# Optimization experiments

Measured on AMD Instinct MI355X. Metric: run time of the kernel, lower is better.

Reference implementation:

```python
import jax, jax.numpy as jnp
import numpy as np

V, E, SH, H = 30000, 1024, 2048, 1024   # vocab, emb_size, ses_hid_size, hid_size
B, T = 64, 50
PAD = 10003
H2 = 2 * H  # GRU hidden size


def setup_inputs() -> dict:
    key = jax.random.key(0)
    ks = jax.random.split(key, 12)
    s = 0.02
    emb_W = jax.random.normal(ks[2], (V, E), jnp.float32) * s
    emb_W = emb_W.at[PAD].set(0.0)  # padding_idx row is zero
    return {
        "ses_encoding": jax.random.normal(ks[0], (B, 1, SH), jnp.float32),
        "x": jax.random.randint(ks[1], (B, T), 0, V),
        "emb_W": emb_W,
        "gru_Wih": jax.random.normal(ks[3], (3 * H2, E), jnp.float32) * s,
        "gru_Whh": jax.random.normal(ks[4], (3 * H2, H2), jnp.float32) * s,
        "gru_bih": jax.random.normal(ks[5], (3 * H2,), jnp.float32) * s,
        "gru_bhh": jax.random.normal(ks[6], (3 * H2,), jnp.float32) * s,
        "lin1_W": jax.random.normal(ks[7], (H, SH), jnp.float32) * s,
        "lin1_b": jax.random.normal(ks[8], (H,), jnp.float32) * s,
        "lin2_W": jax.random.normal(ks[9], (E, H2), jnp.float32) * s,
        "lin2_b": jax.random.normal(ks[10], (E,), jnp.float32) * s,
        "out_W": jax.random.normal(ks[11], (V, E), jnp.float32) * s,
    }


def reference(ses_encoding, x, emb_W, gru_Wih, gru_Whh, gru_bih, gru_bhh,
              lin1_W, lin1_b, lin2_W, lin2_b, out_W):
    # ses_encoding: [B,1,SH] -> tanh(lin1) -> [B,1,H] -> view [1,B,H] -> [B,H]
    ses = jnp.tanh(jnp.einsum('bos,hs->boh', ses_encoding, lin1_W) + lin1_b)
    ses_enc = ses.reshape(B, H)  # [B, H]

    toks = x.T  # [T, B], teacher-forced inputs
    tok_next = jnp.concatenate([x[:, 1:], jnp.zeros((B, 1), x.dtype)], axis=1).T  # [T, B]
    has_next = jnp.arange(T) < (T - 1)  # [T]

    def step(h, xs):
        tok, nxt, hn = xs  # tok: [B]
        emb = jnp.where((tok == PAD)[:, None], 0.0, emb_W[tok])  # [B, E] (dropout=eval identity)
        hcat = jnp.concatenate([h, ses_enc], axis=-1)  # [B, 2H]
        gi = emb @ gru_Wih.T + gru_bih    # [B, 6H]
        gh = hcat @ gru_Whh.T + gru_bhh   # [B, 6H]
        i_r, i_z, i_n = jnp.split(gi, 3, axis=-1)
        h_r, h_z, h_n = jnp.split(gh, 3, axis=-1)
        r = jax.nn.sigmoid(i_r + h_r)
        z = jax.nn.sigmoid(i_z + h_z)
        n = jnp.tanh(i_n + r * h_n)
        h_full = (1.0 - z) * n + z * hcat     # [B, 2H]
        h_next = h_full[:, :H]                # keep first hid_size half
        hid_o = h_full @ lin2_W.T + lin2_b + emb  # [B, E]
        logits = hid_o @ out_W.T              # [B, V]
        logp = jax.nn.log_softmax(logits, axis=-1)
        ll = jnp.where(hn, logp[jnp.arange(B), nxt], 0.0)  # [B]
        return h_next, (logits, ll)

    _, (all_logits, all_ll) = jax.lax.scan(step, ses_enc, (toks, tok_next, has_next))
    dec_o = jnp.transpose(all_logits, (1, 0, 2))  # [B, T, V]
    log_l = jnp.sum(all_ll, axis=0)               # [B]
    return dec_o, log_l
```

## Files before the change

### kernel.cpp

```cpp
#include <hip/hip_runtime.h>
#include <hip/hip_bf16.h>
#include <stdint.h>

#define VV   30000
#define EE   1024
#define SHH  2048
#define HH   1024
#define H2   2048
#define G3   6144
#define BB   64
#define TT   50
#define PADT 10003
#define MM   3200
#define NPAD 30080
#define RBLK 64
#define PNB  (NPAD / 64)

typedef __bf16 bf16;
typedef bf16  bf16x8 __attribute__((ext_vector_type(8)));
typedef bf16  bf16x4v __attribute__((ext_vector_type(4)));
typedef float f32x4 __attribute__((ext_vector_type(4)));

__device__ __forceinline__ void async16(void* lds_base, const void* gsrc) {
    __builtin_amdgcn_global_load_lds(
        (const __attribute__((address_space(1))) void*)gsrc,
        (__attribute__((address_space(3))) void*)lds_base, 16, 0, 0);
}

__device__ __forceinline__ int xcd_swizzle(int lin, int nwg) {
    int q = nwg >> 3, r = nwg & 7;
    int x = lin & 7, o = lin >> 3;
    return (x < r ? x * (q + 1) : r * (q + 1) + (x - r) * q) + o;
}

__device__ __forceinline__ float sigmoidf_(float x) {
    return 1.f / (1.f + __expf(-x));
}

__global__ __launch_bounds__(256) void k_conv(bf16* dst, const float* src, int n) {
    int i = (blockIdx.x * 256 + threadIdx.x) * 4;
    if (i + 3 >= n) return;
    float4 v = *(const float4*)&src[i];
    bf16x4v o; o[0] = (bf16)v.x; o[1] = (bf16)v.y; o[2] = (bf16)v.z; o[3] = (bf16)v.w;
    *(bf16x4v*)&dst[i] = o;
}

__global__ __launch_bounds__(256) void k_conv_outw(bf16* dst, const float* src) {
    int row = blockIdx.x;
    int c = threadIdx.x * 4;
    bf16x4v o;
    if (row < VV) {
        float4 v = *(const float4*)&src[(size_t)row * EE + c];
        o[0] = (bf16)v.x; o[1] = (bf16)v.y; o[2] = (bf16)v.z; o[3] = (bf16)v.w;
    } else {
        o[0] = (bf16)0.f; o[1] = (bf16)0.f; o[2] = (bf16)0.f; o[3] = (bf16)0.f;
    }
    *(bf16x4v*)&dst[(size_t)row * EE + c] = o;
}

__global__ __launch_bounds__(256) void k_conv_whhhi(bf16* dst, const float* whh) {
    int d = blockIdx.x;
    int cblk = d / 192, rem = d % 192, g = rem / 64, s = rem % 64;
    const float* srow = whh + (size_t)(g * H2 + 1024 + cblk * 64 + s) * H2;
    int c = threadIdx.x * 4;
    float4 v = *(const float4*)&srow[c];
    bf16x4v o; o[0] = (bf16)v.x; o[1] = (bf16)v.y; o[2] = (bf16)v.z; o[3] = (bf16)v.w;
    *(bf16x4v*)&dst[(size_t)d * HH + c] = o;
}

__global__ __launch_bounds__(256) void k_embed(const int* x, const float* embW, bf16* out) {
    int i = blockIdx.x;
    int t = i >> 6, b = i & 63;
    int tok = x[b * TT + t];
    int e = threadIdx.x * 4;
    bf16x4v o;
    if (tok == PADT) {
        o[0] = (bf16)0.f; o[1] = (bf16)0.f; o[2] = (bf16)0.f; o[3] = (bf16)0.f;
    } else {
        float4 v = *(const float4*)&embW[(size_t)tok * EE + e];
        o[0] = (bf16)v.x; o[1] = (bf16)v.y; o[2] = (bf16)v.z; o[3] = (bf16)v.w;
    }
    *(bf16x4v*)&out[(size_t)i * EE + e] = o;
}

template<int KIND>
__global__ __launch_bounds__(256)
void sgemm64(const float* __restrict__ A, const float* __restrict__ Bm,
             const float* __restrict__ bias, float* __restrict__ Of, bf16* __restrict__ Ob,
             int N, int K, int lda, int ldb, int koff, int ldo) {
    int n0 = blockIdx.x * 64;
    int tid = threadIdx.x;
    int tr = tid >> 4, tc = tid & 15;
    __shared__ float As[64][33];
    __shared__ float Bs[64][33];
    float acc[4][4] = {};
    for (int k0 = 0; k0 < K; k0 += 32) {
        #pragma unroll
        for (int q = 0; q < 8; ++q) {
            int p = q * 256 + tid; int r = p >> 5, kk = p & 31;
            As[r][kk] = A[(size_t)r * lda + k0 + kk];
            Bs[r][kk] = Bm[(size_t)(n0 + r) * ldb + koff + k0 + kk];
        }
        __syncthreads();
        #pragma unroll
        for (int kk = 0; kk < 32; ++kk) {
            float a4[4], b4[4];
            #pragma unroll
            for (int i = 0; i < 4; i++) a4[i] = As[tr * 4 + i][kk];
            #pragma unroll
            for (int j = 0; j < 4; j++) b4[j] = Bs[tc * 4 + j][kk];
            #pragma unroll
            for (int i = 0; i < 4; i++)
                #pragma unroll
                for (int j = 0; j < 4; j++) acc[i][j] += a4[i] * b4[j];
        }
        __syncthreads();
    }
    #pragma unroll
    for (int i = 0; i < 4; i++)
        #pragma unroll
        for (int j = 0; j < 4; j++) {
            int row = tr * 4 + i, col = n0 + tc * 4 + j;
            float v = acc[i][j] + bias[col];
            if (KIND == 0) {
                v = tanhf(v);
                Of[(size_t)row * N + col] = v;
                Ob[(size_t)row * ldo + col] = (bf16)v;
            } else {
                Of[(size_t)row * N + col] = v;
            }
        }
}

template<int KIND>
__global__ __launch_bounds__(256)
void gemm128(const bf16* __restrict__ A, const bf16* __restrict__ Bm,
             void* __restrict__ Cout, const float* __restrict__ bias,
             const bf16* __restrict__ addend, float* __restrict__ pm,
             float* __restrict__ ps, int N, int K, int lda, int ldb, int Nreal) {
    int nwg = gridDim.x * gridDim.y;
    int lin = blockIdx.y * gridDim.x + blockIdx.x;
    int wg = xcd_swizzle(lin, nwg);
    int bx = wg % gridDim.x, by = wg / gridDim.x;
    const int n0 = bx * 128;
    const int m0 = by * 128;
    const int tid = threadIdx.x;
    const int w = tid >> 6, l = tid & 63;
    const int wr = w >> 1, wc = w & 1;
    __shared__ bf16 As[128 * 32];
    __shared__ bf16 Bs[128 * 32];
    f32x4 acc[4][4] = {};
    const int lrow = l >> 2;
    const int lk = (l & 3) * 8;
    for (int kt = 0; kt < K; kt += 32) {
        #pragma unroll
        for (int q = 0; q < 2; ++q) {
            int ch = w * 2 + q;
            async16(&As[ch * 512], A + (size_t)(m0 + ch * 16 + lrow) * lda + kt + lk);
            async16(&Bs[ch * 512], Bm + (size_t)(n0 + ch * 16 + lrow) * ldb + kt + lk);
        }
        __syncthreads();
        bf16x8 af[4], bfr[4];
        #pragma unroll
        for (int mi = 0; mi < 4; mi++)
            af[mi] = *(const bf16x8*)&As[(wr * 64 + mi * 16 + (l & 15)) * 32 + (l >> 4) * 8];
        #pragma unroll
        for (int ni = 0; ni < 4; ni++)
            bfr[ni] = *(const bf16x8*)&Bs[(wc * 64 + ni * 16 + (l & 15)) * 32 + (l >> 4) * 8];
        #pragma unroll
        for (int mi = 0; mi < 4; mi++)
            #pragma unroll
            for (int ni = 0; ni < 4; ni++)
                acc[mi][ni] = __builtin_amdgcn_mfma_f32_16x16x32_bf16(af[mi], bfr[ni], acc[mi][ni], 0, 0, 0);
        __syncthreads();
    }
    #pragma unroll
    for (int mi = 0; mi < 4; mi++)
        #pragma unroll
        for (int ni = 0; ni < 4; ni++) {
            int row0 = m0 + wr * 64 + mi * 16 + (l >> 4) * 4;
            int col = n0 + wc * 64 + ni * 16 + (l & 15);
            f32x4 v = acc[mi][ni];
            #pragma unroll
            for (int r = 0; r < 4; r++) {
                int rr = row0 + r;
                float xv = v[r];
                if constexpr (KIND == 0 || KIND == 1) xv += bias[col];
                if constexpr (KIND == 1) xv += (float)addend[(size_t)rr * N + col];
                if constexpr (KIND == 2) {
                    if (col < Nreal) {
                        int t = rr >> 6, b = rr & 63;
                        ((float*)Cout)[((size_t)(b * TT + t)) * VV + col] = xv;
                    }
                } else {
                    ((bf16*)Cout)[(size_t)rr * N + col] = (bf16)xv;
                }
            }
        }
    if constexpr (KIND == 2) {
        #pragma unroll
        for (int mi = 0; mi < 4; mi++) {
            #pragma unroll
            for (int r = 0; r < 4; r++) {
                float m = -1e30f, s = 0.f;
                #pragma unroll
                for (int ni = 0; ni < 4; ni++) {
                    int col = n0 + wc * 64 + ni * 16 + (l & 15);
                    if (col < Nreal) {
                        float v = acc[mi][ni][r];
                        float M = fmaxf(m, v);
                        s = s * __expf(m - M) + __expf(v - M);
                        m = M;
                    }
                }
                #pragma unroll
                for (int off = 1; off < 16; off <<= 1) {
                    float m2 = __shfl_xor(m, off);
                    float s2 = __shfl_xor(s, off);
                    float M = fmaxf(m, m2);
                    s = s * __expf(m - M) + s2 * __expf(m2 - M);
                    m = M;
                }
                if ((l & 15) == 0) {
                    int row = m0 + wr * 64 + mi * 16 + (l >> 4) * 4 + r;
                    size_t pidx = (size_t)row * PNB + (n0 >> 6) + wc;
                    pm[pidx] = m; ps[pidx] = s;
                }
            }
        }
    }
}

__global__ __launch_bounds__(384, 1)
void k_rnn(const float* __restrict__ Whh,
           const bf16* __restrict__ gi_b,
           const float* __restrict__ ghs,
           bf16* __restrict__ hfx,
           uint32_t* __restrict__ ctr) {
    const int blk = blockIdx.x;
    const int c0 = blk * 16;
    const int tid = threadIdx.x;
    const int wv = tid >> 6;
    const int l  = tid & 63;
    const int g  = wv >> 1;
    const int mh = wv & 1;
    const int lc = l & 15, lk = l >> 4;
    __shared__ float ghl[3][64][17];

    bf16x8 breg[32];
    {
        const float* wrow = Whh + ((size_t)(g * H2 + c0 + lc)) * H2;
        #pragma unroll
        for (int kt = 0; kt < 32; ++kt) {
            const float* p = wrow + kt * 32 + lk * 8;
            float4 v0 = *(const float4*)p;
            float4 v1 = *(const float4*)(p + 4);
            bf16x8 o;
            o[0] = (bf16)v0.x; o[1] = (bf16)v0.y; o[2] = (bf16)v0.z; o[3] = (bf16)v0.w;
            o[4] = (bf16)v1.x; o[5] = (bf16)v1.y; o[6] = (bf16)v1.z; o[7] = (bf16)v1.w;
            breg[kt] = o;
        }
    }
    float pr[8], pz[8], pn[8];
    if (g == 0) {
        #pragma unroll
        for (int j = 0; j < 8; ++j) {
            int b = mh * 32 + lk * 8 + j;
            size_t base = (size_t)b * G3 + c0 + lc;
            pr[j] = ghs[base];
            pz[j] = ghs[base + H2];
            pn[j] = ghs[base + 2 * H2];
        }
    }

    for (int t = 0; t < TT; ++t) {
        const bf16* arow = hfx + ((size_t)t * BB) * H2;
        bf16 qr[8], qz[8], qn[8];
        if (g == 0) {
            const bf16* gp = gi_b + ((size_t)t * BB) * G3;
            #pragma unroll
            for (int j = 0; j < 8; ++j) {
                int b = mh * 32 + lk * 8 + j;
                size_t base = (size_t)b * G3 + c0 + lc;
                qr[j] = gp[base];
                qz[j] = gp[base + H2];
                qn[j] = gp[base + 2 * H2];
            }
        }
        f32x4 acc0 = {}, acc1 = {};
        #pragma unroll
        for (int kt = 0; kt < 32; ++kt) {
            bf16x8 a0 = *(const bf16x8*)(arow + (size_t)(mh * 32 + lc) * H2 + kt * 32 + lk * 8);
            bf16x8 a1 = *(const bf16x8*)(arow + (size_t)(mh * 32 + 16 + lc) * H2 + kt * 32 + lk * 8);
            acc0 = __builtin_amdgcn_mfma_f32_16x16x32_bf16(a0, breg[kt], acc0, 0, 0, 0);
            acc1 = __builtin_amdgcn_mfma_f32_16x16x32_bf16(a1, breg[kt], acc1, 0, 0, 0);
        }
        #pragma unroll
        for (int r = 0; r < 4; ++r) {
            ghl[g][mh * 32 + lk * 4 + r][lc]      = acc0[r];
            ghl[g][mh * 32 + 16 + lk * 4 + r][lc] = acc1[r];
        }
        __syncthreads();
        if (g == 0) {
            #pragma unroll
            for (int j = 0; j < 8; ++j) {
                int b = mh * 32 + lk * 8 + j;
                float hr = ghl[0][b][lc] + pr[j];
                float hz = ghl[1][b][lc] + pz[j];
                float hn = ghl[2][b][lc] + pn[j];
                float rg = sigmoidf_((float)qr[j] + hr);
                float zg = sigmoidf_((float)qz[j] + hz);
                float ng = tanhf((float)qn[j] + rg * hn);
                float hv = (float)arow[(size_t)b * H2 + c0 + lc];
                float hf = (1.f - zg) * ng + zg * hv;
                hfx[((size_t)(t + 1) * BB + b) * H2 + c0 + lc] = (bf16)hf;
            }
        }
        if (t != TT - 1) {
            __syncthreads();
            if (tid == 0) {
                __hip_atomic_fetch_add(&ctr[t], 1u, __ATOMIC_RELEASE, __HIP_MEMORY_SCOPE_AGENT);
                while (__hip_atomic_load(&ctr[t], __ATOMIC_ACQUIRE, __HIP_MEMORY_SCOPE_AGENT) < RBLK)
                    __builtin_amdgcn_s_sleep(1);
            }
            __syncthreads();
        }
    }
}

__global__ __launch_bounds__(256)
void k_hi(const bf16* __restrict__ hfx_,
          const float* __restrict__ ses_f,
          const bf16* __restrict__ Wrh,
          const bf16* __restrict__ gi_b,
          const float* __restrict__ ghs,
          bf16* __restrict__ hfx_out) {
    const int cblk = blockIdx.x;
    const int t    = blockIdx.y;
    const int tid = threadIdx.x;
    const int w = tid >> 6, l = tid & 63;
    __shared__ bf16 As[64 * 32];
    __shared__ bf16 Bs[192 * 32];
    f32x4 acc[12] = {};
    const int lrow = l >> 2;
    const int lk = (l & 3) * 8;
    const bf16* Abase = hfx_ + ((size_t)t * BB) * H2;
    for (int kt = 0; kt < HH; kt += 32) {
        async16(&As[w * 512], Abase + (size_t)(w * 16 + lrow) * H2 + kt + lk);
        #pragma unroll
        for (int q = 0; q < 3; ++q) {
            int cb = w * 3 + q;
            async16(&Bs[cb * 512], Wrh + (size_t)(cblk * 192 + cb * 16 + lrow) * HH + kt + lk);
        }
        __syncthreads();
        bf16x8 af = *(const bf16x8*)&As[(w * 16 + (l & 15)) * 32 + (l >> 4) * 8];
        #pragma unroll
        for (int j = 0; j < 12; j++) {
            bf16x8 bfj = *(const bf16x8*)&Bs[(j * 16 + (l & 15)) * 32 + (l >> 4) * 8];
            acc[j] = __builtin_amdgcn_mfma_f32_16x16x32_bf16(af, bfj, acc[j], 0, 0, 0);
        }
        __syncthreads();
    }
    #pragma unroll
    for (int jc = 0; jc < 4; jc++) {
        int ch = cblk * 64 + jc * 16 + (l & 15);
        #pragma unroll
        for (int r = 0; r < 4; r++) {
            int b = w * 16 + (l >> 4) * 4 + r;
            size_t gb = (size_t)(t * BB + b) * G3 + 1024 + ch;
            size_t sb = (size_t)b * G3 + 1024 + ch;
            float gr = (float)gi_b[gb];
            float gz = (float)gi_b[gb + H2];
            float gn = (float)gi_b[gb + 2 * H2];
            float hr = acc[jc][r]     + ghs[sb];
            float hz = acc[4 + jc][r] + ghs[sb + H2];
            float hn = acc[8 + jc][r] + ghs[sb + 2 * H2];
            float rg = sigmoidf_(gr + hr);
            float zg = sigmoidf_(gz + hz);
            float ng = tanhf(gn + rg * hn);
            float hv = ses_f[b * HH + ch];
            float hf = (1.f - zg) * ng + zg * hv;
            hfx_out[((size_t)(t + 1) * BB + b) * H2 + HH + ch] = (bf16)hf;
        }
    }
}

__global__ void k_lse(const float* __restrict__ pm, const float* __restrict__ ps,
                      const float* __restrict__ logits, const int* __restrict__ x,
                      float* __restrict__ ll) {
    int row = blockIdx.x;
    int t = row >> 6, b = row & 63;
    int l = threadIdx.x;
    float m = -1e30f, s = 0.f;
    for (int i = l; i < PNB; i += 64) {
        float mi = pm[(size_t)row * PNB + i];
        float si = ps[(size_t)row * PNB + i];
        float M = fmaxf(m, mi);
        s = s * __expf(m - M) + si * __expf(mi - M);
        m = M;
    }
    #pragma unroll
    for (int off = 32; off; off >>= 1) {
        float m2 = __shfl_down(m, off);
        float s2 = __shfl_down(s, off);
        float M = fmaxf(m, m2);
        s = s * __expf(m - M) + s2 * __expf(m2 - M);
        m = M;
    }
    if (l == 0) {
        float v = 0.f;
        if (t < TT - 1) {
            int nxt = x[b * TT + t + 1];
            v = logits[((size_t)(b * TT + t)) * VV + nxt] - (m + __logf(s));
        }
        ll[row] = v;
    }
}

__global__ void k_sumll(const float* __restrict__ ll_ws, float* __restrict__ out) {
    int b = threadIdx.x;
    if (b < BB) {
        float s = 0.f;
        for (int t = 0; t < TT; t++) s += ll_ws[t * BB + b];
        out[b] = s;
    }
}

extern "C" void kernel_launch(void* const* d_in, const int* in_sizes, int n_in,
                              void* d_out, int out_size, void* d_ws, size_t ws_size,
                              hipStream_t stream) {
    const float* ses_encoding = (const float*)d_in[0];
    const int*   x            = (const int*)d_in[1];
    const float* emb_W        = (const float*)d_in[2];
    const float* gru_Wih      = (const float*)d_in[3];
    const float* gru_Whh      = (const float*)d_in[4];
    const float* gru_bih      = (const float*)d_in[5];
    const float* gru_bhh      = (const float*)d_in[6];
    const float* lin1_W       = (const float*)d_in[7];
    const float* lin1_b       = (const float*)d_in[8];
    const float* lin2_W       = (const float*)d_in[9];
    const float* lin2_b       = (const float*)d_in[10];
    const float* out_W        = (const float*)d_in[11];

    char* W = (char*)d_ws;
    size_t off = 0;
    auto take = [&](size_t bytes) { void* p = W + off; off += (bytes + 255) & ~(size_t)255; return p; };

    float* ses_f32 = (float*)take((size_t)BB * HH * 4);
    bf16* Wih_b    = (bf16*)take((size_t)G3 * EE * 2);
    bf16* Wrh_b    = (bf16*)take((size_t)3072 * HH * 2);
    bf16* lin2_b16 = (bf16*)take((size_t)EE * H2 * 2);
    bf16* outW_b   = (bf16*)take((size_t)NPAD * EE * 2);
    bf16* emb_b    = (bf16*)take((size_t)MM * EE * 2);
    bf16* gi_b     = (bf16*)take((size_t)MM * G3 * 2);
    float* ghs     = (float*)take((size_t)BB * G3 * 4);
    bf16* hfx      = (bf16*)take((size_t)(TT + 1) * BB * H2 * 2);
    bf16* hido_b   = (bf16*)take((size_t)MM * EE * 2);
    float* ll_ws   = (float*)take((size_t)MM * 4);
    float* pm      = (float*)take((size_t)MM * PNB * 4);
    float* ps      = (float*)take((size_t)MM * PNB * 4);
    uint32_t* ctr  = (uint32_t*)take((size_t)TT * 4);

    hipMemsetAsync(ctr, 0, TT * 4, stream);

    k_conv<<<(G3 * EE) / 1024, 256, 0, stream>>>(Wih_b, gru_Wih, G3 * EE);
    k_conv<<<(EE * H2) / 1024, 256, 0, stream>>>(lin2_b16, lin2_W, EE * H2);
    k_conv_outw<<<NPAD, 256, 0, stream>>>(outW_b, out_W);
    k_conv_whhhi<<<3072, 256, 0, stream>>>(Wrh_b, gru_Whh);
    k_embed<<<MM, 256, 0, stream>>>(x, emb_W, emb_b);

    sgemm64<0><<<HH / 64, 256, 0, stream>>>(ses_encoding, lin1_W, lin1_b, ses_f32, hfx,
                                            HH, SHH, SHH, SHH, 0, H2);
    sgemm64<1><<<G3 / 64, 256, 0, stream>>>(ses_f32, gru_Whh, gru_bhh, ghs, nullptr,
                                            G3, HH, HH, H2, HH, 0);

    gemm128<0><<<dim3(G3 / 128, MM / 128), 256, 0, stream>>>(
        emb_b, Wih_b, gi_b, gru_bih, nullptr, nullptr, nullptr, G3, EE, EE, EE, 0);

    k_rnn<<<RBLK, 384, 0, stream>>>(gru_Whh, gi_b, ghs, hfx, ctr);

    k_hi<<<dim3(16, TT), 256, 0, stream>>>(hfx, ses_f32, Wrh_b, gi_b, ghs, hfx);

    gemm128<1><<<dim3(EE / 128, MM / 128), 256, 0, stream>>>(
        hfx + (size_t)BB * H2, lin2_b16, hido_b, lin2_b, emb_b, nullptr, nullptr,
        EE, H2, H2, H2, 0);

    gemm128<2><<<dim3(NPAD / 128, MM / 128), 256, 0, stream>>>(
        hido_b, outW_b, d_out, nullptr, nullptr, pm, ps, NPAD, EE, EE, EE, VV);

    k_lse<<<MM, 64, 0, stream>>>(pm, ps, (const float*)d_out, x, ll_ws);
    k_sumll<<<1, 64, 0, stream>>>(ll_ws, (float*)d_out + (size_t)BB * TT * VV);
}
```

Baseline: 1.651 ms.

## Stage recurrent hidden state into swizzled LDS and spread GRU gate epilogue

Each recurrent step now copies the 64x1024 bf16 hidden-state tile into a 128KB XOR-swizzled LDS buffer with async global-to-LDS loads. The MFMA A-operands and the previous-h value in the gate update are then read from LDS instead of each wave re-reading global memory. The gate epilogue is spread over four waves with four rows each instead of two waves with eight. The grid barrier spin now uses relaxed loads followed by an acquire fence. This trades an extra block-wide sync per step and a near-full LDS allocation for less redundant L2 traffic on the serial critical path.

```diff
diff --git a/kernel.cpp b/kernel.cpp
--- a/kernel.cpp
+++ b/kernel.cpp
@@ -245,6 +245,7 @@
     const int g  = wv >> 1;
     const int mh = wv & 1;
     const int lc = l & 15, lk = l >> 4;
+    __shared__ char h_lds[131072];
     __shared__ float ghl[3][64][17];
 
     bf16x8 breg[32];
@@ -261,37 +262,55 @@
             breg[kt] = o;
         }
     }
-    float pr[8], pz[8], pn[8];
-    if (g == 0) {
-        #pragma unroll
-        for (int j = 0; j < 8; ++j) {
-            int b = mh * 32 + lk * 8 + j;
+    float pr[4], pz[4], pn[4];
+    if (wv < 4) {
+        #pragma unroll
+        for (int r = 0; r < 4; ++r) {
+            int b = wv * 16 + lk * 4 + r;
             size_t base = (size_t)b * G3 + c0 + lc;
-            pr[j] = ghs[base];
-            pz[j] = ghs[base + H2];
-            pn[j] = ghs[base + 2 * H2];
+            pr[r] = ghs[base];
+            pz[r] = ghs[base + H2];
+            pn[r] = ghs[base + 2 * H2];
         }
     }
 
     for (int t = 0; t < TT; ++t) {
-        const bf16* arow = hfx + ((size_t)t * BB) * H2;
-        bf16 qr[8], qz[8], qn[8];
-        if (g == 0) {
+        {
+            const char* hbase = (const char*)(hfx + (size_t)t * BB * H2);
+            #pragma unroll
+            for (int i = 0; i < 22; ++i) {
+                int wo = i * 6144 + wv * 1024;
+                if (wo < 131072) {
+                    int o = wo + l * 16;
+                    int row = o >> 11, cb = o & 2047;
+                    const char* src = hbase + row * 4096 + (cb ^ ((row & 7) << 4));
+                    async16(h_lds + wo, src);
+                }
+            }
+        }
+        __syncthreads();
+
+        bf16 qr[4], qz[4], qn[4];
+        if (wv < 4) {
             const bf16* gp = gi_b + ((size_t)t * BB) * G3;
             #pragma unroll
-            for (int j = 0; j < 8; ++j) {
-                int b = mh * 32 + lk * 8 + j;
+            for (int r = 0; r < 4; ++r) {
+                int b = wv * 16 + lk * 4 + r;
                 size_t base = (size_t)b * G3 + c0 + lc;
-                qr[j] = gp[base];
-                qz[j] = gp[base + H2];
-                qn[j] = gp[base + 2 * H2];
-            }
-        }
+                qr[r] = gp[base];
+                qz[r] = gp[base + H2];
+                qn[r] = gp[base + 2 * H2];
+            }
+        }
+
         f32x4 acc0 = {}, acc1 = {};
+        const int r0 = mh * 32 + lc, r1 = r0 + 16;
+        const int sw = (lc & 7) << 4;
         #pragma unroll
         for (int kt = 0; kt < 32; ++kt) {
-            bf16x8 a0 = *(const bf16x8*)(arow + (size_t)(mh * 32 + lc) * H2 + kt * 32 + lk * 8);
-            bf16x8 a1 = *(const bf16x8*)(arow + (size_t)(mh * 32 + 16 + lc) * H2 + kt * 32 + lk * 8);
+            int cbyte = kt * 64 + lk * 16;
+            bf16x8 a0 = *(const bf16x8*)(h_lds + ((r0 * 2048 + cbyte) ^ sw));
+            bf16x8 a1 = *(const bf16x8*)(h_lds + ((r1 * 2048 + cbyte) ^ sw));
             acc0 = __builtin_amdgcn_mfma_f32_16x16x32_bf16(a0, breg[kt], acc0, 0, 0, 0);
             acc1 = __builtin_amdgcn_mfma_f32_16x16x32_bf16(a1, breg[kt], acc1, 0, 0, 0);
         }
@@ -301,27 +320,31 @@
             ghl[g][mh * 32 + 16 + lk * 4 + r][lc] = acc1[r];
         }
         __syncthreads();
-        if (g == 0) {
-            #pragma unroll
-            for (int j = 0; j < 8; ++j) {
-                int b = mh * 32 + lk * 8 + j;
-                float hr = ghl[0][b][lc] + pr[j];
-                float hz = ghl[1][b][lc] + pz[j];
-                float hn = ghl[2][b][lc] + pn[j];
-                float rg = sigmoidf_((float)qr[j] + hr);
-                float zg = sigmoidf_((float)qz[j] + hz);
-                float ng = tanhf((float)qn[j] + rg * hn);
-                float hv = (float)arow[(size_t)b * H2 + c0 + lc];
+
+        if (wv < 4) {
+            #pragma unroll
+            for (int r = 0; r < 4; ++r) {
+                int b = wv * 16 + lk * 4 + r;
+                float hr = ghl[0][b][lc] + pr[r];
+                float hz = ghl[1][b][lc] + pz[r];
+                float hn = ghl[2][b][lc] + pn[r];
+                float rg = sigmoidf_((float)qr[r] + hr);
+                float zg = sigmoidf_((float)qz[r] + hz);
+                float ng = tanhf((float)qn[r] + rg * hn);
+                int hvb = (b * 2048 + (c0 + lc) * 2) ^ ((b & 7) << 4);
+                float hv = (float)*(const bf16*)(h_lds + hvb);
                 float hf = (1.f - zg) * ng + zg * hv;
                 hfx[((size_t)(t + 1) * BB + b) * H2 + c0 + lc] = (bf16)hf;
             }
         }
+
         if (t != TT - 1) {
             __syncthreads();
             if (tid == 0) {
                 __hip_atomic_fetch_add(&ctr[t], 1u, __ATOMIC_RELEASE, __HIP_MEMORY_SCOPE_AGENT);
-                while (__hip_atomic_load(&ctr[t], __ATOMIC_ACQUIRE, __HIP_MEMORY_SCOPE_AGENT) < RBLK)
-                    __builtin_amdgcn_s_sleep(1);
+                while (__hip_atomic_load(&ctr[t], __ATOMIC_RELAXED, __HIP_MEMORY_SCOPE_AGENT) < RBLK)
+                    __builtin_amdgcn_s_sleep(2);
+                __builtin_amdgcn_fence(__ATOMIC_ACQUIRE, "agent");
             }
             __syncthreads();
         }
```

Measured after the change: 1.565 ms. 1.06x faster.
